# Optimization experiments

Measured on AMD Instinct MI355X. Metric: run time of the kernel, lower is better.

## Reference

```python
import jax, jax.numpy as jnp
import numpy as np

SHIFT, REDUCE = 1, 2
B, L, E, H = 128, 64, 512, 512
T = 2 * L - 1  # valid binary-parse transition sequence length


def _make_transitions(rng):
    # Random *valid* shift-reduce sequences: L shifts, L-1 reduces, stack ends at 1.
    trans = np.zeros((B, T), dtype=np.int32)
    for b in range(B):
        stack, buf = 0, L
        for t in range(T):
            ops_left = T - t
            can_shift = buf > 0 and stack < ops_left
            can_reduce = stack >= 2
            if can_shift and can_reduce:
                act = SHIFT if rng.random() < 0.5 else REDUCE
            elif can_shift:
                act = SHIFT
            else:
                act = REDUCE
            if act == SHIFT:
                buf -= 1; stack += 1
            else:
                stack -= 1
            trans[b, t] = act
    return trans


def setup_inputs() -> dict:
    key = jax.random.key(0)
    k1, k2, k3, k4 = jax.random.split(key, 4)
    sentence = jax.random.normal(k1, (B, L, E), dtype=jnp.float32)
    transitions = jnp.asarray(_make_transitions(np.random.default_rng(0)))
    W_word = jax.random.normal(k2, (E, 2 * H), dtype=jnp.float32) / np.sqrt(E).astype(np.float32)
    b_word = jnp.zeros((2 * H,), dtype=jnp.float32)
    W_left = jax.random.normal(k3, (H, 5 * H), dtype=jnp.float32) / np.sqrt(H).astype(np.float32)
    W_right = jax.random.normal(k4, (H, 5 * H), dtype=jnp.float32) / np.sqrt(H).astype(np.float32)
    b_reduce = jnp.zeros((5 * H,), dtype=jnp.float32)
    return {"sentence": sentence, "transitions": transitions, "W_word": W_word,
            "b_word": b_word, "W_left": W_left, "W_right": W_right, "b_reduce": b_reduce}


def reference(sentence, transitions, W_word, b_word, W_left, W_right, b_reduce):
    Bx, Lx, _ = sentence.shape
    Hx = W_left.shape[0]
    Tx = transitions.shape[1]
    # word projection (no_batch_norm=True, dropout=0 in this config)
    out = sentence @ W_word + b_word                      # [B, L, 2H]
    h_buf, c_buf = jnp.split(out, 2, axis=2)              # buffers, popped front-to-back
    rows = jnp.arange(Bx)
    ops_left_seq = jnp.arange(Tx, 0, -1, dtype=jnp.int32)
    init = (jnp.zeros((Bx, Lx, Hx), out.dtype),           # stack h
            jnp.zeros((Bx, Lx, Hx), out.dtype),           # stack c
            jnp.zeros((Bx,), jnp.int32),                  # stack ptr
            jnp.zeros((Bx,), jnp.int32))                  # buffer ptr

    def step(carry, xs):
        sh, sc, sp, bp = carry
        act, ops = xs
        act = jnp.where(sp > ops, REDUCE, act)            # forced reduce (discrete stack)
        is_red = act == REDUCE
        is_shf = act == SHIFT
        r_idx = jnp.clip(sp - 1, 0, Lx - 1)
        l_idx = jnp.clip(sp - 2, 0, Lx - 1)
        hl, cl = sh[rows, l_idx], sc[rows, l_idx]
        hr, cr = sh[rows, r_idx], sc[rows, r_idx]
        # TreeLSTM Reduce cell
        gates = hl @ W_left + hr @ W_right + b_reduce     # [B, 5H]
        g, i, f1, f2, o = jnp.split(gates, 5, axis=1)
        c_red = jnp.tanh(g) * jax.nn.sigmoid(i) + jax.nn.sigmoid(f1) * cl + jax.nn.sigmoid(f2) * cr
        h_red = jax.nn.sigmoid(o) * jnp.tanh(c_red)
        b_idx = jnp.clip(bp, 0, Lx - 1)
        h_shf, c_shf = h_buf[rows, b_idx], c_buf[rows, b_idx]
        w_idx = jnp.where(is_red, l_idx, jnp.clip(sp, 0, Lx - 1))
        h_cur, c_cur = sh[rows, w_idx], sc[rows, w_idx]
        m_red, m_shf = is_red[:, None], is_shf[:, None]
        wh = jnp.where(m_red, h_red, jnp.where(m_shf, h_shf, h_cur))
        wc = jnp.where(m_red, c_red, jnp.where(m_shf, c_shf, c_cur))
        sh = sh.at[rows, w_idx].set(wh)
        sc = sc.at[rows, w_idx].set(wc)
        sp = sp + is_shf.astype(jnp.int32) - is_red.astype(jnp.int32)
        bp = bp + is_shf.astype(jnp.int32)
        return (sh, sc, sp, bp), None

    (sh, sc, sp, bp), _ = jax.lax.scan(step, init, (transitions.T, ops_left_seq))
    return sh[rows, jnp.clip(sp - 1, 0, Lx - 1)]          # [B, H] top of each stack
```

## Files before the change

### kernel.cpp

```cpp
#include <hip/hip_runtime.h>
#include <hip/hip_bf16.h>


#define Bn 128
#define Ln 64
#define En 512
#define Hn 512
#define Tn 127
#define LEAF_ROWS (Bn*Ln)
#define NODE_ROWS (Bn*(Ln-1))
#define TOT_ROWS (LEAF_ROWS+NODE_ROWS)
#define NLVL 64
#define NXCD 8
#define CAPX 512
#define NBLK 512
#define FPAD 16
#define MAXRANK 96
#define SPIN_CAP (1<<22)
#define GATE_STRIDE (512*1024)
#define WLDS_BYTES 65536
#define PART_BYTES (4*3*16*20*4)
#define DYN_BYTES (WLDS_BYTES + PART_BYTES)

#define OFF_CENSUS 0
#define OFF_RANK   (OFF_CENSUS + NXCD*FPAD)
#define OFF_SFLAG  (OFF_RANK + NBLK*FPAD)
#define OFF_SGEN   (OFF_SFLAG + NBLK*FPAD)
#define OFF_FX     (OFF_SGEN + FPAD)
#define OFF_GX     (OFF_FX + NXCD*MAXRANK*FPAD)
#define BAR_INTS   (OFF_GX + NXCD*FPAD)

typedef __attribute__((ext_vector_type(8))) short bf16x8;
typedef __attribute__((ext_vector_type(4))) float f32x4;

static __device__ __forceinline__ float bf2f(unsigned short u){
  unsigned v = ((unsigned)u) << 16;
  float f; __builtin_memcpy(&f, &v, 4); return f;
}
static __device__ __forceinline__ unsigned short f2bf(float f){
  unsigned u; __builtin_memcpy(&u, &f, 4);
  u = u + 0x7FFFu + ((u >> 16) & 1u);
  return (unsigned short)(u >> 16);
}
static __device__ __forceinline__ float sigm(float x){
  return 1.0f / (1.0f + __expf(-x));
}
static __device__ __forceinline__ float tanh_fast(float x){
  x = fminf(fmaxf(x, -15.0f), 15.0f);
  float t = __expf(2.0f * x);
  return (t - 1.0f) / (t + 1.0f);
}
static __device__ __forceinline__ int xcc_id(){
  unsigned v;
  asm volatile("s_getreg_b32 %0, hwreg(HW_REG_XCC_ID)" : "=s"(v));
  return (int)(v & 7);
}

static __device__ __forceinline__ void xcd_barrier(int* bar, int x, int rank, int nx, int epoch){
  __syncthreads();
  int* fx = bar + OFF_FX + x * MAXRANK * FPAD;
  int* gx = bar + OFF_GX + x * FPAD;
  int nxl = min(nx, MAXRANK);
  if (rank == 0){
    for (int i = threadIdx.x + 1; i < nxl; i += 256){
      int c = 0;
      while (__hip_atomic_load(&fx[i * FPAD], __ATOMIC_RELAXED, __HIP_MEMORY_SCOPE_AGENT) < epoch && c < SPIN_CAP){
        ++c;
      }
    }
    __syncthreads();
    if (threadIdx.x == 0)
      __hip_atomic_store(gx, epoch, __ATOMIC_RELAXED, __HIP_MEMORY_SCOPE_AGENT);
  } else {
    if (threadIdx.x == 0){
      __hip_atomic_store(&fx[rank * FPAD], epoch, __ATOMIC_RELAXED, __HIP_MEMORY_SCOPE_AGENT);
      int c = 0;
      while (__hip_atomic_load(gx, __ATOMIC_RELAXED, __HIP_MEMORY_SCOPE_AGENT) < epoch && c < SPIN_CAP){
        __builtin_amdgcn_s_sleep(1); ++c;
      }
    }
    __syncthreads();
  }
  asm volatile("" ::: "memory");
}


__global__ void cvt_vec4(const float4* __restrict__ x, ushort4* __restrict__ y, int n4){
  int i = blockIdx.x * 256 + threadIdx.x;
  if (i < n4){
    float4 v = x[i];
    ushort4 o;
    o.x = f2bf(v.x); o.y = f2bf(v.y); o.z = f2bf(v.z); o.w = f2bf(v.w);
    y[i] = o;
  }
}

__global__ void transpose_cvt(const float* __restrict__ src, unsigned short* __restrict__ dstT,
                              int CS, int DS, int koff){
  __shared__ float tile[32][33];
  int c0 = blockIdx.x * 32, r0 = blockIdx.y * 32;
  int tx = threadIdx.x, ty = threadIdx.y;
  for (int i = ty; i < 32; i += 8) tile[i][tx] = src[(size_t)(r0 + i) * CS + c0 + tx];
  __syncthreads();
  for (int i = ty; i < 32; i += 8)
    dstT[(size_t)(c0 + i) * DS + koff + r0 + tx] = f2bf(tile[tx][i]);
}

__global__ void precompute_ctrl(const int* __restrict__ trans,
                                int* __restrict__ srcL, int* __restrict__ srcR,
                                int* __restrict__ dstv, int* __restrict__ cnt,
                                int* __restrict__ outsrc, int* __restrict__ bar){
  __shared__ int stk[Bn][Ln + 1];
  __shared__ int scnt[NXCD * NLVL];
  __shared__ int smaxl[NXCD];
  int b = threadIdx.x;
  for (int i = b; i < NXCD * NLVL; i += 128) scnt[i] = 0;
  if (b < NXCD) smaxl[b] = 0;
  for (int i = b; i < BAR_INTS; i += 128) bar[i] = 0;
  __syncthreads();
  int x = b & 7;
  int sp = 0, bp = 0, nodecnt = 0;
  int act_next = trans[b * Tn];
  for (int t = 0; t < Tn; t++){
    int act = act_next;
    if (t + 1 < Tn) act_next = trans[b * Tn + t + 1];
    int ops = Tn - t;
    if (sp > ops) act = 2;
    if (act == 2){
      int R = stk[b][sp - 1], L = stk[b][sp - 2];
      int lvl = max(R >> 20, L >> 20) + 1;
      int slot = atomicAdd(&scnt[x * NLVL + lvl], 1);
      int base = (x * NLVL + lvl) * CAPX + slot;
      srcL[base] = (L & 0xFFFFF) * Hn;
      srcR[base] = (R & 0xFFFFF) * Hn;
      int noderow = LEAF_ROWS + b * (Ln - 1) + nodecnt;
      dstv[base] = noderow * Hn;
      stk[b][sp - 2] = noderow | (lvl << 20);
      sp -= 1; nodecnt++;
    } else {
      stk[b][sp] = b * Ln + min(bp, Ln - 1);
      sp += 1; bp += 1;
    }
  }
  int root = stk[b][max(sp - 1, 0)];
  outsrc[b] = (root & 0xFFFFF) * Hn;
  atomicMax(&smaxl[x], root >> 20);
  __syncthreads();
  for (int i = b; i < NXCD * NLVL; i += 128) cnt[i] = scnt[i];
  if (b < NXCD) cnt[NXCD * NLVL + b] = smaxl[b];
}

__global__ __launch_bounds__(256) void word_gemm(
    const unsigned short* __restrict__ SB, const unsigned short* __restrict__ WwT,
    const float* __restrict__ b_word,
    unsigned short* __restrict__ HB, float* __restrict__ CF){
  int mt = blockIdx.x;
  int nt = blockIdx.y;
  int tid = threadIdx.x, w = tid >> 6, lane = tid & 63;
  int wm = w >> 1, wn = w & 1;
  int rc = lane & 15, lg = lane >> 4;
  const unsigned short* ap0 = SB + (size_t)(mt * 64 + wm * 32 + rc) * En + lg * 8;
  const unsigned short* ap1 = ap0 + (size_t)16 * En;
  const unsigned short* bp0 = WwT + (size_t)(nt * 128 + wn * 64 + rc) * En + lg * 8;
  f32x4 acc[2][4];
  #pragma unroll
  for (int h = 0; h < 2; h++)
    #pragma unroll
    for (int nb = 0; nb < 4; nb++) acc[h][nb] = (f32x4){0.f,0.f,0.f,0.f};

  bf16x8 aS0[3], aS1[3], bS[4][3];
  #pragma unroll
  for (int s = 0; s < 2; s++){
    aS0[s] = *(const bf16x8*)(ap0 + s * 32);
    aS1[s] = *(const bf16x8*)(ap1 + s * 32);
    #pragma unroll
    for (int nb = 0; nb < 4; nb++)
      bS[nb][s] = *(const bf16x8*)(bp0 + (size_t)nb * 16 * En + s * 32);
  }
  #pragma unroll
  for (int j = 0; j < 16; ++j){
    const int cur = j % 3, n2 = (j + 2) % 3;
    if (j < 14){
      int kn = (j + 2) * 32;
      aS0[n2] = *(const bf16x8*)(ap0 + kn);
      aS1[n2] = *(const bf16x8*)(ap1 + kn);
      #pragma unroll
      for (int nb = 0; nb < 4; nb++)
        bS[nb][n2] = *(const bf16x8*)(bp0 + (size_t)nb * 16 * En + kn);
    }
    #pragma unroll
    for (int nb = 0; nb < 4; nb++){
      acc[0][nb] = __builtin_amdgcn_mfma_f32_16x16x32_bf16(aS0[cur], bS[nb][cur], acc[0][nb], 0, 0, 0);
      acc[1][nb] = __builtin_amdgcn_mfma_f32_16x16x32_bf16(aS1[cur], bS[nb][cur], acc[1][nb], 0, 0, 0);
    }
  }
  #pragma unroll
  for (int nb = 0; nb < 4; nb++){
    int col = nt * 128 + wn * 64 + nb * 16 + rc;
    float bw = b_word[col];
    #pragma unroll
    for (int h = 0; h < 2; h++){
      #pragma unroll
      for (int q = 0; q < 4; q++){
        int row = mt * 64 + wm * 32 + h * 16 + lg * 4 + q;
        float v = acc[h][nb][q] + bw;
        if (col < Hn) HB[(size_t)row * Hn + col] = f2bf(v);
        else          CF[(size_t)row * Hn + (col - Hn)] = v;
      }
    }
  }
}

template<bool LDSB>
static __device__ __forceinline__ void tile64(
    int u0, int t, int nr, const int* __restrict__ sL, const int* __restrict__ sR,
    const int* __restrict__ dl,
    unsigned short* __restrict__ HB, float* __restrict__ CF,
    const unsigned short* __restrict__ WT, const float* __restrict__ b_red,
    const unsigned short* __restrict__ wlds, int rc, int lg)
{
  int base = t * 64;
  int offL[4], offR[4];
  #pragma unroll
  for (int m = 0; m < 4; m++){
    int i = min(base + m * 16 + rc, nr - 1);
    offL[m] = sL[i]; offR[m] = sR[i];
  }
  f32x4 acc[5][4];
  #pragma unroll
  for (int g = 0; g < 5; g++)
    #pragma unroll
    for (int m = 0; m < 4; m++) acc[g][m] = (f32x4){0.f,0.f,0.f,0.f};

  int bswz = (rc & 7) << 3;
  const unsigned short* gb = WT + (size_t)(u0 + rc) * 1024 + lg * 8;

  bf16x8 a_cur[4], b_cur[3];
  #pragma unroll
  for (int m = 0; m < 4; m++) a_cur[m] = *(const bf16x8*)(HB + offL[m] + lg * 8);
  #pragma unroll
  for (int g = 0; g < 3; g++)
    b_cur[g] = *(const bf16x8*)(gb + (size_t)(g + 2) * GATE_STRIDE);

  #pragma unroll 4
  for (int j = 0; j < 32; ++j){
    bf16x8 a_nxt[4], b_nxt[3];
    if (j < 31){
      int kn = (j + 1) * 32 + lg * 8;
      #pragma unroll
      for (int m = 0; m < 4; m++){
        const unsigned short* ap = (j + 1 < 16) ? (HB + offL[m] + kn) : (HB + offR[m] + (kn - 512));
        a_nxt[m] = *(const bf16x8*)ap;
      }
      #pragma unroll
      for (int g = 0; g < 3; g++)
        b_nxt[g] = *(const bf16x8*)(gb + (size_t)(g + 2) * GATE_STRIDE + (j + 1) * 32);
    }
    int k = j * 32 + lg * 8;
    #pragma unroll
    for (int g = 0; g < 2; g++){
      bf16x8 bb;
      if (LDSB) bb = *(const bf16x8*)&wlds[(size_t)(g * 16 + rc) * 1024 + (k ^ bswz)];
      else      bb = *(const bf16x8*)(gb + (size_t)g * GATE_STRIDE + j * 32);
      #pragma unroll
      for (int m = 0; m < 4; m++)
        acc[g][m] = __builtin_amdgcn_mfma_f32_16x16x32_bf16(a_cur[m], bb, acc[g][m], 0, 0, 0);
    }
    #pragma unroll
    for (int g = 0; g < 3; g++){
      #pragma unroll
      for (int m = 0; m < 4; m++)
        acc[g + 2][m] = __builtin_amdgcn_mfma_f32_16x16x32_bf16(a_cur[m], b_cur[g], acc[g + 2][m], 0, 0, 0);
    }
    #pragma unroll
    for (int m = 0; m < 4; m++) a_cur[m] = a_nxt[m];
    #pragma unroll
    for (int g = 0; g < 3; g++) b_cur[g] = b_nxt[g];
  }
  int colu = u0 + rc;
  float bs[5];
  #pragma unroll
  for (int g = 0; g < 5; g++) bs[g] = b_red[g * Hn + colu];
  #pragma unroll
  for (int m = 0; m < 4; m++){
    #pragma unroll
    for (int q = 0; q < 4; q++){
      int i = base + m * 16 + lg * 4 + q;
      if (i < nr){
        int oL = sL[i], oR = sR[i], oD = dl[i];
        float gv = tanh_fast(acc[0][m][q] + bs[0]);
        float iv = sigm(acc[1][m][q] + bs[1]);
        float f1 = sigm(acc[2][m][q] + bs[2]);
        float f2 = sigm(acc[3][m][q] + bs[3]);
        float ov = sigm(acc[4][m][q] + bs[4]);
        float cl = __builtin_nontemporal_load(CF + oL + colu);
        float cr = __builtin_nontemporal_load(CF + oR + colu);
        float cv = gv * iv + f1 * cl + f2 * cr;
        float hv = ov * tanh_fast(cv);
        __builtin_nontemporal_store(cv, CF + oD + colu);
        HB[oD + colu] = f2bf(hv);
      }
    }
  }
}

static __device__ __forceinline__ void tile16(
    int u0, int t, int nr, const int* __restrict__ sL, const int* __restrict__ sR,
    const int* __restrict__ dl,
    unsigned short* __restrict__ HB, float* __restrict__ CF,
    const unsigned short* __restrict__ WT, const float* __restrict__ b_red,
    const unsigned short* __restrict__ wlds, float (*part)[3][16][20],
    int tid, int w, int rc, int lg,
    bool up, int pre_offA, int pre_oL, int pre_oR, int pre_oD)
{
  int base = t * 16;
  int er = tid >> 4, eu = tid & 15;
  int offA, oL, oR, oD;
  if (up){
    offA = pre_offA; oL = pre_oL; oR = pre_oR; oD = pre_oD;
  } else {
    int i0 = min(base + rc, nr - 1);
    offA = (w >= 2) ? sR[i0] : sL[i0];
    int ie = min(base + er, nr - 1);
    oL = sL[ie]; oR = sR[ie]; oD = dl[ie];
  }
  int colu = u0 + eu;
  float cl = __builtin_nontemporal_load(CF + oL + colu);
  float cr = __builtin_nontemporal_load(CF + oR + colu);

  int k0 = w * 256;
  int abase = (w >= 2) ? (k0 - 512) : k0;
  const unsigned short* ap = HB + offA + abase + lg * 8;
  int bswz = (rc & 7) << 3;
  const unsigned short* gb = WT + (size_t)(u0 + rc) * 1024;

  f32x4 acc[5];
  #pragma unroll
  for (int g = 0; g < 5; g++) acc[g] = (f32x4){0.f,0.f,0.f,0.f};

  bf16x8 aS[3], bS[3][3];
  #pragma unroll
  for (int s = 0; s < 2; s++){
    aS[s] = *(const bf16x8*)(ap + s * 32);
    #pragma unroll
    for (int g = 0; g < 3; g++)
      bS[g][s] = *(const bf16x8*)(gb + (size_t)(g + 2) * GATE_STRIDE + k0 + s * 32 + lg * 8);
  }
  #pragma unroll
  for (int j = 0; j < 8; ++j){
    const int cur = j % 3, n2 = (j + 2) % 3;
    if (j < 6){
      aS[n2] = *(const bf16x8*)(ap + (j + 2) * 32);
      #pragma unroll
      for (int g = 0; g < 3; g++)
        bS[g][n2] = *(const bf16x8*)(gb + (size_t)(g + 2) * GATE_STRIDE + k0 + (j + 2) * 32 + lg * 8);
    }
    int k = k0 + j * 32 + lg * 8;
    #pragma unroll
    for (int g = 0; g < 2; g++){
      bf16x8 bb = *(const bf16x8*)&wlds[(size_t)(g * 16 + rc) * 1024 + (k ^ bswz)];
      acc[g] = __builtin_amdgcn_mfma_f32_16x16x32_bf16(aS[cur], bb, acc[g], 0, 0, 0);
    }
    #pragma unroll
    for (int g = 0; g < 3; g++)
      acc[g + 2] = __builtin_amdgcn_mfma_f32_16x16x32_bf16(aS[cur], bS[g][cur], acc[g + 2], 0, 0, 0);
  }
  float sg[5];
  #pragma unroll
  for (int g = 0; g < 3; g++)
    #pragma unroll
    for (int q = 0; q < 4; q++) part[w][g][lg * 4 + q][rc] = acc[g][q];
  __syncthreads();
  #pragma unroll
  for (int g = 0; g < 3; g++)
    sg[g] = part[0][g][er][eu] + part[1][g][er][eu] + part[2][g][er][eu] + part[3][g][er][eu];
  __syncthreads();
  #pragma unroll
  for (int g = 0; g < 2; g++)
    #pragma unroll
    for (int q = 0; q < 4; q++) part[w][g][lg * 4 + q][rc] = acc[3 + g][q];
  __syncthreads();
  #pragma unroll
  for (int g = 0; g < 2; g++)
    sg[3 + g] = part[0][g][er][eu] + part[1][g][er][eu] + part[2][g][er][eu] + part[3][g][er][eu];

  int i = base + er;
  if (i < nr){
    float gv = tanh_fast(sg[0] + b_red[colu]);
    float iv = sigm(sg[1] + b_red[Hn + colu]);
    float f1 = sigm(sg[2] + b_red[2 * Hn + colu]);
    float f2 = sigm(sg[3] + b_red[3 * Hn + colu]);
    float ov = sigm(sg[4] + b_red[4 * Hn + colu]);
    float cv = gv * iv + f1 * cl + f2 * cr;
    float hv = ov * tanh_fast(cv);
    __builtin_nontemporal_store(cv, CF + oD + colu);
    HB[oD + colu] = f2bf(hv);
  }
  __syncthreads();
}

extern __shared__ char dynbuf[];

__global__ __launch_bounds__(256, 2) void tree_kernel(
    unsigned short* __restrict__ HB, float* __restrict__ CF,
    const unsigned short* __restrict__ WT, const float* __restrict__ b_red,
    const int* __restrict__ srcL, const int* __restrict__ srcR,
    const int* __restrict__ dstv, const int* __restrict__ cnt,
    const int* __restrict__ outsrc, float* __restrict__ out, int* bar){
  unsigned short* wlds = (unsigned short*)dynbuf;
  float (*part)[3][16][20] = (float(*)[3][16][20])(dynbuf + WLDS_BYTES);
  int bid = blockIdx.x;
  int tid = threadIdx.x, w = tid >> 6, lane = tid & 63;
  int rc = lane & 15, lg = lane >> 4;
  int er = tid >> 4;

  int x = xcc_id();
  if (tid == 0){
    int r = __hip_atomic_fetch_add(&bar[OFF_CENSUS + x * FPAD], 1,
                                   __ATOMIC_RELAXED, __HIP_MEMORY_SCOPE_AGENT);
    __hip_atomic_store(&bar[OFF_RANK + bid * FPAD], r, __ATOMIC_RELAXED, __HIP_MEMORY_SCOPE_AGENT);
  }
  __syncthreads();
  int rank = min(__hip_atomic_load(&bar[OFF_RANK + bid * FPAD], __ATOMIC_RELAXED, __HIP_MEMORY_SCOPE_AGENT),
                 MAXRANK - 1);
  int ub = rank & 31;
  int u0 = ub * 16;

  for (int gg = tid; gg < 4096; gg += 256){
    int row = gg >> 7;
    int k = (gg & 127) * 8;
    int u = row & 15, g = row >> 4;
    bf16x8 v = *(const bf16x8*)(WT + (size_t)(g * 512 + u0 + u) * 1024 + k);
    int kx = k ^ ((u & 7) << 3);
    *(bf16x8*)&wlds[(size_t)row * 1024 + kx] = v;
  }
  __syncthreads();

  {
    int* sfl  = bar + OFF_SFLAG;
    int* sgen = bar + OFF_SGEN;
    if (bid == 0){
      for (int i = tid; i < NBLK; i += 256){
        if (i){
          int c = 0;
          while (__hip_atomic_load(&sfl[i * FPAD], __ATOMIC_RELAXED, __HIP_MEMORY_SCOPE_AGENT) == 0 && c < SPIN_CAP){
            __builtin_amdgcn_s_sleep(1); ++c;
          }
        }
      }
      __syncthreads();
      if (tid == 0) __hip_atomic_store(sgen, 1, __ATOMIC_RELAXED, __HIP_MEMORY_SCOPE_AGENT);
    } else {
      if (tid == 0){
        __hip_atomic_store(&sfl[bid * FPAD], 1, __ATOMIC_RELAXED, __HIP_MEMORY_SCOPE_AGENT);
        int c = 0;
        while (__hip_atomic_load(sgen, __ATOMIC_RELAXED, __HIP_MEMORY_SCOPE_AGENT) == 0 && c < SPIN_CAP){
          __builtin_amdgcn_s_sleep(2); ++c;
        }
      }
      __syncthreads();
    }
  }
  int nx = max(__hip_atomic_load(&bar[OFF_CENSUS + x * FPAD], __ATOMIC_RELAXED, __HIP_MEMORY_SCOPE_AGENT), 1);

  int maxlvl = cnt[NXCD * NLVL + x];
  int epoch = 1;
  int pre_offA = 0, pre_oL = 0, pre_oR = 0, pre_oD = 0;
  bool have_pre = false;
  for (int lvl = 1; lvl <= maxlvl; ++lvl, ++epoch){
    int nr = cnt[x * NLVL + lvl];
    const int* sL = srcL + (x * NLVL + lvl) * CAPX;
    const int* sR = srcR + (x * NLVL + lvl) * CAPX;
    const int* dl = dstv + (x * NLVL + lvl) * CAPX;
    int stripe = rank >> 5;
    if (nr > 0){
      if (nx >= 32){
        int nstr = (nx - 1 - ub) / 32 + 1;
        if (nr >= 128){
          int ntl = (nr + 63) >> 6;
          for (int t = stripe * 4 + w; t < ntl; t += nstr * 4)
            tile64<true>(u0, t, nr, sL, sR, dl, HB, CF, WT, b_red, wlds, rc, lg);
        } else {
          int ntl16 = (nr + 15) >> 4;
          for (int t = stripe; t < ntl16; t += nstr)
            tile16(u0, t, nr, sL, sR, dl, HB, CF, WT, b_red, wlds, part, tid, w, rc, lg,
                   have_pre && (t == stripe), pre_offA, pre_oL, pre_oR, pre_oD);
        }
      } else {
        int ntl = (nr + 63) >> 6;
        int nwv = nx * 4, wid = rank * 4 + w;
        int ntask = ntl * 32;
        for (int task = wid; task < ntask; task += nwv)
          tile64<false>((task / ntl) * 16, task % ntl, nr, sL, sR, dl, HB, CF, WT, b_red, wlds, rc, lg);
      }
    }
    have_pre = false;
    if (lvl < maxlvl && nx >= 32){
      int nr2 = cnt[x * NLVL + lvl + 1];
      if (nr2 > 0 && nr2 < 128){
        const int* sL2 = srcL + (x * NLVL + lvl + 1) * CAPX;
        const int* sR2 = srcR + (x * NLVL + lvl + 1) * CAPX;
        const int* dl2 = dstv + (x * NLVL + lvl + 1) * CAPX;
        int ntl2 = (nr2 + 15) >> 4;
        if (stripe < ntl2){
          int i0 = min(stripe * 16 + rc, nr2 - 1);
          pre_offA = (w >= 2) ? sR2[i0] : sL2[i0];
          int ie = min(stripe * 16 + er, nr2 - 1);
          pre_oL = sL2[ie]; pre_oR = sR2[ie]; pre_oD = dl2[ie];
          have_pre = true;
        }
      }
    }
    xcd_barrier(bar, x, rank, nx, epoch);
  }

  for (int j = rank; j < 16; j += min(nx, MAXRANK)){
    int b = x + 8 * j;
    int src = outsrc[b];
    out[b * Hn + tid]       = bf2f(HB[src + tid]);
    out[b * Hn + tid + 256] = bf2f(HB[src + tid + 256]);
  }
}

extern "C" void kernel_launch(void* const* d_in, const int* in_sizes, int n_in,
                              void* d_out, int out_size, void* d_ws, size_t ws_size,
                              hipStream_t stream){
  (void)in_sizes; (void)n_in; (void)out_size; (void)ws_size;
  const float* sentence = (const float*)d_in[0];
  const int*   trans    = (const int*)d_in[1];
  const float* W_word   = (const float*)d_in[2];
  const float* b_word   = (const float*)d_in[3];
  const float* W_left   = (const float*)d_in[4];
  const float* W_right  = (const float*)d_in[5];
  const float* b_red    = (const float*)d_in[6];

  char* ws = (char*)d_ws;
  size_t off = 0;
  auto alloc = [&](size_t bytes) -> void* {
    void* p = ws + off;
    off += (bytes + 255) & ~((size_t)255);
    return p;
  };
  unsigned short* HB  = (unsigned short*)alloc((size_t)TOT_ROWS * Hn * 2);
  float*          CF  = (float*)alloc((size_t)TOT_ROWS * Hn * 4);
  unsigned short* WT  = (unsigned short*)alloc((size_t)2560 * 1024 * 2);
  unsigned short* SB  = (unsigned short*)alloc((size_t)LEAF_ROWS * En * 2);
  unsigned short* WwT = (unsigned short*)alloc((size_t)1024 * En * 2);
  int* srcL   = (int*)alloc((size_t)NXCD * NLVL * CAPX * 4);
  int* srcR   = (int*)alloc((size_t)NXCD * NLVL * CAPX * 4);
  int* dstv   = (int*)alloc((size_t)NXCD * NLVL * CAPX * 4);
  int* cnt    = (int*)alloc((size_t)(NXCD * NLVL + NXCD) * 4);
  int* outsrc = (int*)alloc((size_t)Bn * 4);
  int* bar    = (int*)alloc((size_t)BAR_INTS * 4);
  float* outp = (float*)d_out;

  hipFuncSetAttribute(reinterpret_cast<const void*>(tree_kernel),
                      hipFuncAttributeMaxDynamicSharedMemorySize, DYN_BYTES);

  cvt_vec4<<<(LEAF_ROWS * En / 4) / 256, 256, 0, stream>>>((const float4*)sentence, (ushort4*)SB, LEAF_ROWS * En / 4);
  transpose_cvt<<<dim3(1024 / 32, En / 32), dim3(32, 8), 0, stream>>>(W_word, WwT, 1024, En, 0);
  transpose_cvt<<<dim3(2560 / 32, Hn / 32), dim3(32, 8), 0, stream>>>(W_left, WT, 2560, 1024, 0);
  transpose_cvt<<<dim3(2560 / 32, Hn / 32), dim3(32, 8), 0, stream>>>(W_right, WT, 2560, 1024, 512);
  precompute_ctrl<<<1, 128, 0, stream>>>(trans, srcL, srcR, dstv, cnt, outsrc, bar);
  word_gemm<<<dim3(128, 8), 256, 0, stream>>>(SB, WwT, b_word, HB, CF);
  tree_kernel<<<NBLK, 256, DYN_BYTES, stream>>>(HB, CF, WT, b_red, srcL, srcR, dstv, cnt, outsrc, outp, bar);
}
```

Measured before the change: 669.8 us.

## Flatten XCD barrier to all-to-all polling and restructure GEMM operand prefetch

The per-XCD barrier drops the leader gather/broadcast in favour of every block publishing its epoch and polling all peers' flags directly, with a short spin before sleeping. This removes one round trip through the leader on each tree level, at the cost of more atomic polling traffic. Separately, the word GEMM moves from a triple-buffered to a double-buffered register prefetch, and the tree reduce step loads all A and B fragments up front before the MFMA loop. The tree kernel's occupancy hint changes from a launch_bounds min-blocks value to amdgpu_waves_per_eu(2,2). Together these trade register pressure for more memory-level parallelism.

New measurement: 726.1 us. 1.08x slower.

```diff
diff --git a/kernel.cpp b/kernel.cpp
--- a/kernel.cpp
+++ b/kernel.cpp
@@ -27,8 +27,7 @@
 #define OFF_SFLAG  (OFF_RANK + NBLK*FPAD)
 #define OFF_SGEN   (OFF_SFLAG + NBLK*FPAD)
 #define OFF_FX     (OFF_SGEN + FPAD)
-#define OFF_GX     (OFF_FX + NXCD*MAXRANK*FPAD)
-#define BAR_INTS   (OFF_GX + NXCD*FPAD)
+#define BAR_INTS   (OFF_FX + NXCD*MAXRANK*FPAD)
 
 typedef __attribute__((ext_vector_type(8))) short bf16x8;
 typedef __attribute__((ext_vector_type(4))) float f32x4;
@@ -59,28 +58,18 @@
 static __device__ __forceinline__ void xcd_barrier(int* bar, int x, int rank, int nx, int epoch){
   __syncthreads();
   int* fx = bar + OFF_FX + x * MAXRANK * FPAD;
-  int* gx = bar + OFF_GX + x * FPAD;
+  if (threadIdx.x == 0)
+    __hip_atomic_store(&fx[rank * FPAD], epoch, __ATOMIC_RELAXED, __HIP_MEMORY_SCOPE_AGENT);
   int nxl = min(nx, MAXRANK);
-  if (rank == 0){
-    for (int i = threadIdx.x + 1; i < nxl; i += 256){
-      int c = 0;
-      while (__hip_atomic_load(&fx[i * FPAD], __ATOMIC_RELAXED, __HIP_MEMORY_SCOPE_AGENT) < epoch && c < SPIN_CAP){
-        ++c;
-      }
-    }
-    __syncthreads();
-    if (threadIdx.x == 0)
-      __hip_atomic_store(gx, epoch, __ATOMIC_RELAXED, __HIP_MEMORY_SCOPE_AGENT);
-  } else {
-    if (threadIdx.x == 0){
-      __hip_atomic_store(&fx[rank * FPAD], epoch, __ATOMIC_RELAXED, __HIP_MEMORY_SCOPE_AGENT);
-      int c = 0;
-      while (__hip_atomic_load(gx, __ATOMIC_RELAXED, __HIP_MEMORY_SCOPE_AGENT) < epoch && c < SPIN_CAP){
-        __builtin_amdgcn_s_sleep(1); ++c;
-      }
-    }
-    __syncthreads();
-  }
+  if ((int)threadIdx.x < nxl){
+    int c = 0;
+    while (__hip_atomic_load(&fx[threadIdx.x * FPAD], __ATOMIC_RELAXED, __HIP_MEMORY_SCOPE_AGENT) < epoch
+           && c < SPIN_CAP){
+      if (c > 8) __builtin_amdgcn_s_sleep(1);
+      ++c;
+    }
+  }
+  __syncthreads();
   asm volatile("" ::: "memory");
 }
 
@@ -168,31 +157,31 @@
     #pragma unroll
     for (int nb = 0; nb < 4; nb++) acc[h][nb] = (f32x4){0.f,0.f,0.f,0.f};
 
-  bf16x8 aS0[3], aS1[3], bS[4][3];
-  #pragma unroll
-  for (int s = 0; s < 2; s++){
-    aS0[s] = *(const bf16x8*)(ap0 + s * 32);
-    aS1[s] = *(const bf16x8*)(ap1 + s * 32);
-    #pragma unroll
-    for (int nb = 0; nb < 4; nb++)
-      bS[nb][s] = *(const bf16x8*)(bp0 + (size_t)nb * 16 * En + s * 32);
-  }
+  bf16x8 a0c = *(const bf16x8*)ap0;
+  bf16x8 a1c = *(const bf16x8*)ap1;
+  bf16x8 bc[4];
+  #pragma unroll
+  for (int nb = 0; nb < 4; nb++) bc[nb] = *(const bf16x8*)(bp0 + (size_t)nb * 16 * En);
+
   #pragma unroll
   for (int j = 0; j < 16; ++j){
-    const int cur = j % 3, n2 = (j + 2) % 3;
-    if (j < 14){
-      int kn = (j + 2) * 32;
-      aS0[n2] = *(const bf16x8*)(ap0 + kn);
-      aS1[n2] = *(const bf16x8*)(ap1 + kn);
+    bf16x8 a0n, a1n, bn[4];
+    if (j < 15){
+      int kn = (j + 1) * 32;
+      a0n = *(const bf16x8*)(ap0 + kn);
+      a1n = *(const bf16x8*)(ap1 + kn);
       #pragma unroll
       for (int nb = 0; nb < 4; nb++)
-        bS[nb][n2] = *(const bf16x8*)(bp0 + (size_t)nb * 16 * En + kn);
+        bn[nb] = *(const bf16x8*)(bp0 + (size_t)nb * 16 * En + kn);
     }
     #pragma unroll
     for (int nb = 0; nb < 4; nb++){
-      acc[0][nb] = __builtin_amdgcn_mfma_f32_16x16x32_bf16(aS0[cur], bS[nb][cur], acc[0][nb], 0, 0, 0);
-      acc[1][nb] = __builtin_amdgcn_mfma_f32_16x16x32_bf16(aS1[cur], bS[nb][cur], acc[1][nb], 0, 0, 0);
-    }
+      acc[0][nb] = __builtin_amdgcn_mfma_f32_16x16x32_bf16(a0c, bc[nb], acc[0][nb], 0, 0, 0);
+      acc[1][nb] = __builtin_amdgcn_mfma_f32_16x16x32_bf16(a1c, bc[nb], acc[1][nb], 0, 0, 0);
+    }
+    a0c = a0n; a1c = a1n;
+    #pragma unroll
+    for (int nb = 0; nb < 4; nb++) bc[nb] = bn[nb];
   }
   #pragma unroll
   for (int nb = 0; nb < 4; nb++){
@@ -334,36 +323,31 @@
   int bswz = (rc & 7) << 3;
   const unsigned short* gb = WT + (size_t)(u0 + rc) * 1024;
 
+  bf16x8 aF[8];
+  #pragma unroll
+  for (int j = 0; j < 8; ++j) aF[j] = *(const bf16x8*)(ap + j * 32);
+  bf16x8 bF[8][3];
+  #pragma unroll
+  for (int j = 0; j < 8; ++j)
+    #pragma unroll
+    for (int g = 0; g < 3; g++)
+      bF[j][g] = *(const bf16x8*)(gb + (size_t)(g + 2) * GATE_STRIDE + k0 + j * 32 + lg * 8);
+
   f32x4 acc[5];
   #pragma unroll
   for (int g = 0; g < 5; g++) acc[g] = (f32x4){0.f,0.f,0.f,0.f};
 
-  bf16x8 aS[3], bS[3][3];
-  #pragma unroll
-  for (int s = 0; s < 2; s++){
-    aS[s] = *(const bf16x8*)(ap + s * 32);
-    #pragma unroll
-    for (int g = 0; g < 3; g++)
-      bS[g][s] = *(const bf16x8*)(gb + (size_t)(g + 2) * GATE_STRIDE + k0 + s * 32 + lg * 8);
-  }
   #pragma unroll
   for (int j = 0; j < 8; ++j){
-    const int cur = j % 3, n2 = (j + 2) % 3;
-    if (j < 6){
-      aS[n2] = *(const bf16x8*)(ap + (j + 2) * 32);
-      #pragma unroll
-      for (int g = 0; g < 3; g++)
-        bS[g][n2] = *(const bf16x8*)(gb + (size_t)(g + 2) * GATE_STRIDE + k0 + (j + 2) * 32 + lg * 8);
-    }
     int k = k0 + j * 32 + lg * 8;
     #pragma unroll
     for (int g = 0; g < 2; g++){
       bf16x8 bb = *(const bf16x8*)&wlds[(size_t)(g * 16 + rc) * 1024 + (k ^ bswz)];
-      acc[g] = __builtin_amdgcn_mfma_f32_16x16x32_bf16(aS[cur], bb, acc[g], 0, 0, 0);
+      acc[g] = __builtin_amdgcn_mfma_f32_16x16x32_bf16(aF[j], bb, acc[g], 0, 0, 0);
     }
     #pragma unroll
     for (int g = 0; g < 3; g++)
-      acc[g + 2] = __builtin_amdgcn_mfma_f32_16x16x32_bf16(aS[cur], bS[g][cur], acc[g + 2], 0, 0, 0);
+      acc[g + 2] = __builtin_amdgcn_mfma_f32_16x16x32_bf16(aF[j], bF[j][g], acc[g + 2], 0, 0, 0);
   }
   float sg[5];
   #pragma unroll
@@ -401,7 +385,9 @@
 
 extern __shared__ char dynbuf[];
 
-__global__ __launch_bounds__(256, 2) void tree_kernel(
+__global__ __launch_bounds__(256)
+__attribute__((amdgpu_waves_per_eu(2, 2)))
+void tree_kernel(
     unsigned short* __restrict__ HB, float* __restrict__ CF,
     const unsigned short* __restrict__ WT, const float* __restrict__ b_red,
     const int* __restrict__ srcL, const int* __restrict__ srcR,
```
